# Optimization experiments

Hardware: AMD Instinct MI355X
Metric: run time of the kernel (lower is better)

## Reference

```python
import jax, jax.numpy as jnp
import numpy as np

B, C, H, W = 4, 8, 1024, 1024


def setup_inputs() -> dict:
    key = jax.random.key(0)
    k1, k2, k3 = jax.random.split(key, 3)
    outs = jax.random.normal(k1, (B, C, H, W), dtype=jnp.float32)
    # soft target maps in [0,1) (one-hot in practice; math identical, mask all-True)
    targets = jax.random.uniform(k2, (B, C, H, W), dtype=jnp.float32)
    class_weight = jax.random.uniform(k3, (C,), dtype=jnp.float32)
    return {"outs": outs, "targets": targets, "class_weight": class_weight,
            "logits_input": 1}


def reference(outs, targets, class_weight, logits_input):
    # forward(): optional log_softmax over class dim, then flatten spatial dims
    x = jax.nn.log_softmax(outs, axis=1) if logits_input else outs
    b, c = x.shape[0], x.shape[1]
    x = x.reshape(b, c, -1)           # [B, C, N]
    t = targets.reshape(b, c, -1)     # [B, C, N]
    # CELoss with ignore=-1: mask = targets != ignore, per-(batch,class) masked mean
    mask = t != -1.0                  # [B, C, N] (all True for prob targets)
    cnt = mask.sum(axis=-1).astype(x.dtype)                     # [B, C]
    per_bc = -(t * x * class_weight[None, :, None] * mask).sum(axis=-1) / cnt
    # loss per batch = sum over classes / C ; nan -> 1.0 ; mean over batch
    loss_b = jnp.nan_to_num(per_bc.mean(axis=1), nan=1.0)       # [B]
    return loss_b.mean()
```

## Files before the change

### kernel.cpp

```cpp
#include <hip/hip_runtime.h>

#define B_   4
#define C_   8
#define LOGN 20
#define NPOS (1u << LOGN)
#define G_   4

typedef float v4f __attribute__((ext_vector_type(4)));

__global__ __launch_bounds__(256) void ce_partial_kernel(
    const float* __restrict__ outs,
    const float* __restrict__ targets,
    const float* __restrict__ cw,
    const int*   __restrict__ flag_p,
    float* __restrict__ partials)
{
    const int flag = *flag_p;
    float w[C_];
#pragma unroll
    for (int c = 0; c < C_; ++c) w[c] = cw[c];

    const int i0 = blockIdx.x * 1024 + threadIdx.x;
    const int b  = i0 >> 18;
    const int n0 = (i0 << 2) & (NPOS - 1);
    const float* __restrict__ obase = outs    + (((size_t)b * C_) << LOGN) + n0;
    const float* __restrict__ tbase = targets + (((size_t)b * C_) << LOGN) + n0;

    v4f dot[G_], swt[G_], E[G_];
#pragma unroll
    for (int g = 0; g < G_; ++g) { dot[g] = (v4f)(0.f); swt[g] = (v4f)(0.f); E[g] = (v4f)(0.f); }

#pragma unroll
    for (int c = 0; c < C_; ++c) {
        v4f o[G_], t[G_];
        const float* oc_p = obase + ((size_t)c << LOGN);
        const float* tc_p = tbase + ((size_t)c << LOGN);
#pragma unroll
        for (int g = 0; g < G_; ++g) {
            o[g] = __builtin_nontemporal_load((const v4f*)(oc_p + (g << 10)));
            t[g] = __builtin_nontemporal_load((const v4f*)(tc_p + (g << 10)));
        }
#pragma unroll
        for (int g = 0; g < G_; ++g) {
            const v4f oc = o[g];
            const v4f wt = w[c] * t[g];
            dot[g] += wt * oc;
            swt[g] += wt;
            E[g].x += __expf(oc.x);
            E[g].y += __expf(oc.y);
            E[g].z += __expf(oc.z);
            E[g].w += __expf(oc.w);
        }
    }

    float acc = 0.0f;
    if (flag) {
#pragma unroll
        for (int g = 0; g < G_; ++g) {
            v4f lse;
            lse.x = __logf(E[g].x);
            lse.y = __logf(E[g].y);
            lse.z = __logf(E[g].z);
            lse.w = __logf(E[g].w);
            const v4f r = dot[g] - lse * swt[g];
            acc += r.x + r.y + r.z + r.w;
        }
    } else {
#pragma unroll
        for (int g = 0; g < G_; ++g)
            acc += dot[g].x + dot[g].y + dot[g].z + dot[g].w;
    }

#pragma unroll
    for (int off = 32; off > 0; off >>= 1) acc += __shfl_down(acc, off, 64);

    __shared__ float sm[4];
    const int lane = threadIdx.x & 63;
    const int wave = threadIdx.x >> 6;
    if (lane == 0) sm[wave] = acc;
    __syncthreads();
    if (threadIdx.x == 0) {
        partials[blockIdx.x] = sm[0] + sm[1] + sm[2] + sm[3];
    }
}

__global__ __launch_bounds__(256) void ce_final_kernel(
    const float* __restrict__ partials, int nblocks,
    float* __restrict__ out, float scale)
{
    float acc = 0.0f;
    for (int i = threadIdx.x; i < nblocks; i += 256) acc += partials[i];
#pragma unroll
    for (int off = 32; off > 0; off >>= 1) acc += __shfl_down(acc, off, 64);
    __shared__ float sm[4];
    const int lane = threadIdx.x & 63;
    const int wave = threadIdx.x >> 6;
    if (lane == 0) sm[wave] = acc;
    __syncthreads();
    if (threadIdx.x == 0) {
        out[0] = (sm[0] + sm[1] + sm[2] + sm[3]) * scale;
    }
}

extern "C" void kernel_launch(void* const* d_in, const int* in_sizes, int n_in,
                              void* d_out, int out_size, void* d_ws, size_t ws_size,
                              hipStream_t stream) {
    const float* outs    = (const float*)d_in[0];
    const float* targets = (const float*)d_in[1];
    const float* cw      = (const float*)d_in[2];
    const int*   flag    = (const int*)d_in[3];
    float* partials = (float*)d_ws;
    float* out      = (float*)d_out;

    const int blocks = (B_ * (int)NPOS) / 4 / (256 * G_);

    ce_partial_kernel<<<blocks, 256, 0, stream>>>(outs, targets, cw, flag, partials);

    const float scale = -1.0f / (float)((size_t)B_ * C_ * NPOS);
    ce_final_kernel<<<1, 256, 0, stream>>>(partials, blocks, out, scale);
}
```

Measured before the change: 258.7 us.

## Give each wave a contiguous chunk and load two class planes at once

Each wavefront now owns a contiguous 1024-element span of one spatial slice, so its four vector loads per plane cover adjacent 1KB segments instead of strided 4KB offsets. The class loop is processed in pairs, issuing 16 nontemporal vector loads before a scheduling barrier to raise memory-level parallelism. The launch bounds add a min-blocks hint. The aim is more bytes in flight per wave and better DRAM locality, at the cost of higher register pressure from doubling the live load buffers.

```diff
diff --git a/kernel.cpp b/kernel.cpp
--- a/kernel.cpp
+++ b/kernel.cpp
@@ -8,7 +8,7 @@
 
 typedef float v4f __attribute__((ext_vector_type(4)));
 
-__global__ __launch_bounds__(256) void ce_partial_kernel(
+__global__ __launch_bounds__(256, 4) void ce_partial_kernel(
     const float* __restrict__ outs,
     const float* __restrict__ targets,
     const float* __restrict__ cw,
@@ -20,36 +20,45 @@
 #pragma unroll
     for (int c = 0; c < C_; ++c) w[c] = cw[c];
 
-    const int i0 = blockIdx.x * 1024 + threadIdx.x;
-    const int b  = i0 >> 18;
-    const int n0 = (i0 << 2) & (NPOS - 1);
-    const float* __restrict__ obase = outs    + (((size_t)b * C_) << LOGN) + n0;
-    const float* __restrict__ tbase = targets + (((size_t)b * C_) << LOGN) + n0;
+    const int wave = threadIdx.x >> 6;
+    const int lane = threadIdx.x & 63;
+    const int wb = (blockIdx.x * 4 + wave) * 1024;
+    const int b  = wb >> LOGN;
+    const int n  = wb & (NPOS - 1);
+    const size_t base = (((size_t)b * C_) << LOGN) + (size_t)n + (size_t)(lane << 2);
+    const float* __restrict__ obase = outs    + base;
+    const float* __restrict__ tbase = targets + base;
 
     v4f dot[G_], swt[G_], E[G_];
 #pragma unroll
     for (int g = 0; g < G_; ++g) { dot[g] = (v4f)(0.f); swt[g] = (v4f)(0.f); E[g] = (v4f)(0.f); }
 
 #pragma unroll
-    for (int c = 0; c < C_; ++c) {
-        v4f o[G_], t[G_];
-        const float* oc_p = obase + ((size_t)c << LOGN);
-        const float* tc_p = tbase + ((size_t)c << LOGN);
+    for (int cp = 0; cp < C_ / 2; ++cp) {
+        const int c0 = 2 * cp, c1 = 2 * cp + 1;
+        const float* o0 = obase + ((size_t)c0 << LOGN);
+        const float* t0 = tbase + ((size_t)c0 << LOGN);
+        const float* o1 = obase + ((size_t)c1 << LOGN);
+        const float* t1 = tbase + ((size_t)c1 << LOGN);
+        v4f oa[G_], ta[G_], ob[G_], tb[G_];
 #pragma unroll
         for (int g = 0; g < G_; ++g) {
-            o[g] = __builtin_nontemporal_load((const v4f*)(oc_p + (g << 10)));
-            t[g] = __builtin_nontemporal_load((const v4f*)(tc_p + (g << 10)));
+            oa[g] = __builtin_nontemporal_load((const v4f*)(o0 + (g << 8)));
+            ta[g] = __builtin_nontemporal_load((const v4f*)(t0 + (g << 8)));
+            ob[g] = __builtin_nontemporal_load((const v4f*)(o1 + (g << 8)));
+            tb[g] = __builtin_nontemporal_load((const v4f*)(t1 + (g << 8)));
         }
+        __builtin_amdgcn_sched_barrier(0);
 #pragma unroll
         for (int g = 0; g < G_; ++g) {
-            const v4f oc = o[g];
-            const v4f wt = w[c] * t[g];
-            dot[g] += wt * oc;
-            swt[g] += wt;
-            E[g].x += __expf(oc.x);
-            E[g].y += __expf(oc.y);
-            E[g].z += __expf(oc.z);
-            E[g].w += __expf(oc.w);
+            const v4f oc0 = oa[g], wt0 = w[c0] * ta[g];
+            dot[g] += wt0 * oc0;  swt[g] += wt0;
+            E[g].x += __expf(oc0.x); E[g].y += __expf(oc0.y);
+            E[g].z += __expf(oc0.z); E[g].w += __expf(oc0.w);
+            const v4f oc1 = ob[g], wt1 = w[c1] * tb[g];
+            dot[g] += wt1 * oc1;  swt[g] += wt1;
+            E[g].x += __expf(oc1.x); E[g].y += __expf(oc1.y);
+            E[g].z += __expf(oc1.z); E[g].w += __expf(oc1.w);
         }
     }
 
@@ -75,8 +84,6 @@
     for (int off = 32; off > 0; off >>= 1) acc += __shfl_down(acc, off, 64);
 
     __shared__ float sm[4];
-    const int lane = threadIdx.x & 63;
-    const int wave = threadIdx.x >> 6;
     if (lane == 0) sm[wave] = acc;
     __syncthreads();
     if (threadIdx.x == 0) {
@@ -112,7 +119,7 @@
     float* partials = (float*)d_ws;
     float* out      = (float*)d_out;
 
-    const int blocks = (B_ * (int)NPOS) / 4 / (256 * G_);
+    const int blocks = (B_ * (int)NPOS) / 4096;
 
     ce_partial_kernel<<<blocks, 256, 0, stream>>>(outs, targets, cw, flag, partials);
 
```

New measurement: 317.4 us. 1.23x slower.
